# Kernel tuning notes

Measured on AMD Instinct MI355X. Metric: run time of the kernel, lower is better.

The kernel has to match this reference:

```python
import jax, jax.numpy as jnp
import numpy as np

M = 128        # out_features (= in_features here)
N = 20000      # num_node
E = 320000     # num edges (avg degree 16)
KAPPA = 0.99   # inf-norm projection radius (A_rho = 1.0)


def project_linf(W, v):
    """Project each row of W onto the L1 ball of radius v (=> ||W||_inf <= v),
    matching IGNN's projection_norm_inf (rows with L1 norm <= v are untouched)."""
    absW = jnp.abs(W)
    row_l1 = absW.sum(axis=1)
    u = jnp.sort(absW, axis=1)[:, ::-1]          # descending per row
    cssv = jnp.cumsum(u, axis=1) - v
    ind = jnp.arange(1, W.shape[1] + 1, dtype=W.dtype)
    rho = jnp.sum(u * ind > cssv, axis=1)        # support size, >=1 when row_l1 > v
    theta = cssv[jnp.arange(W.shape[0]), rho - 1] / rho.astype(W.dtype)
    proj = jnp.sign(W) * jnp.maximum(absW - theta[:, None], 0.0)
    return jnp.where((row_l1 > v)[:, None], proj, W)


def spmm_right(Xm, rows, cols, vals, n):
    """Compute Xm @ A for sparse A with A[rows[e], cols[e]] = vals[e]; Xm: [m, n]."""
    g = Xm[:, rows] * vals                                    # [m, E]
    return jax.ops.segment_sum(g.T, cols, num_segments=n).T  # [m, n]


def setup_inputs() -> dict:
    key = jax.random.key(0)
    ks = jax.random.split(key, 7)
    stdv = 1.0 / np.sqrt(M)
    X_0 = jax.random.normal(ks[0], (M, N), jnp.float32)
    U = jax.random.normal(ks[1], (M, N), jnp.float32)
    W = jax.random.uniform(ks[2], (M, M), jnp.float32, -stdv, stdv)
    Omega_1 = jax.random.uniform(ks[3], (M, M), jnp.float32, -stdv, stdv)
    A_rows = jax.random.randint(ks[4], (E,), 0, N)
    A_cols = jax.random.randint(ks[5], (E,), 0, N)
    # positive, roughly degree-normalized adjacency values
    A_values = jax.random.uniform(ks[6], (E,), jnp.float32) / 16.0
    return dict(X_0=X_0, U=U, W=W, Omega_1=Omega_1, A_values=A_values,
                A_rows=A_rows, A_cols=A_cols, fw_mitr=30)


def reference(X_0, U, W, Omega_1, A_values, A_rows, A_cols, fw_mitr):
    n = X_0.shape[1]
    # self.W = projection_norm_inf(self.W, kappa / A_rho), A_rho = 1.0
    Wp = project_linf(W, KAPPA)
    # b_Omega = (A^T @ (U^T @ Omega_1^T))^T = (Omega_1 @ U) @ A
    B = spmm_right(Omega_1 @ U, A_rows, A_cols, A_values, n)  # [m, n]
    # ImplicitFunction fixed-point iteration: X <- phi(W @ X @ A + B), phi = relu
    def step(X, _):
        X_new = jax.nn.relu(spmm_right(Wp @ X, A_rows, A_cols, A_values, n) + B)
        return X_new, None
    X, _ = jax.lax.scan(step, X_0, None, length=fw_mitr)
    return X
```

## Files before the change

kernel.cpp:

```cpp
#include <hip/hip_runtime.h>

#define MDIM 128
#define NCOL 20000
#define NEDGE 320000
#define NITER 30
#define FKAPPA 0.99f

typedef unsigned int uint;
typedef unsigned short ushort;
typedef __attribute__((ext_vector_type(8))) short short8;
typedef __attribute__((ext_vector_type(4))) float f32x4;

__device__ __forceinline__ float bf2f(ushort b){
    uint u = ((uint)b) << 16;
    return __builtin_bit_cast(float, u);
}
__device__ __forceinline__ ushort f2bf(float f){
    uint u = __builtin_bit_cast(uint, f);
    uint r = (u + 0x7fffu + ((u >> 16) & 1u)) >> 16;
    return (ushort)r;
}

__global__ void k_zero(int* __restrict__ p){
    int i = blockIdx.x * 256 + threadIdx.x;
    if (i < 2 * NCOL) p[i] = 0;
}

__global__ void k_hist(const int* __restrict__ cols, int* __restrict__ cnt){
    int e = blockIdx.x * 256 + threadIdx.x;
    if (e < NEDGE) atomicAdd(&cnt[cols[e]], 1);
}

__global__ void k_scan(const int* __restrict__ cnt, int* __restrict__ start){
    __shared__ int lds[256];
    const int SEG = (NCOL + 255) / 256;
    int t = threadIdx.x;
    int lo = t * SEG;
    int hi = min(lo + SEG, NCOL);
    int s = 0;
    for (int i = lo; i < hi; ++i) s += cnt[i];
    lds[t] = s;
    __syncthreads();
    for (int off = 1; off < 256; off <<= 1){
        int v = (t >= off) ? lds[t - off] : 0;
        __syncthreads();
        lds[t] += v;
        __syncthreads();
    }
    int run = (t > 0) ? lds[t - 1] : 0;
    for (int i = lo; i < hi; ++i){ start[i] = run; run += cnt[i]; }
    if (hi == NCOL && lo < NCOL) start[NCOL] = run;
}

__global__ void k_scatter(const int* __restrict__ rows, const int* __restrict__ cols,
                          const float* __restrict__ vals, const int* __restrict__ start,
                          int* __restrict__ cursor, uint2* __restrict__ edges){
    int e = blockIdx.x * 256 + threadIdx.x;
    if (e < NEDGE){
        int c = cols[e];
        int p = start[c] + atomicAdd(&cursor[c], 1);
        edges[p] = make_uint2((uint)rows[e], __builtin_bit_cast(uint, vals[e]));
    }
}

__global__ void k_project(const float* __restrict__ W, ushort* __restrict__ Wp){
    int row = blockIdx.x * 4 + (threadIdx.x >> 6);
    int l = threadIdx.x & 63;
    const float* wr = W + row * MDIM;
    float w0 = wr[l], w1 = wr[l + 64];
    float a0 = fabsf(w0), a1 = fabsf(w1);
    float s = a0 + a1, mx = fmaxf(a0, a1);
    for (int off = 32; off; off >>= 1){
        s += __shfl_xor(s, off);
        mx = fmaxf(mx, __shfl_xor(mx, off));
    }
    if (s > FKAPPA){
        float tlo = 0.f, thi = mx;
        for (int it = 0; it < 48; ++it){
            float th = 0.5f * (tlo + thi);
            float f = fmaxf(a0 - th, 0.f) + fmaxf(a1 - th, 0.f);
            for (int off = 32; off; off >>= 1) f += __shfl_xor(f, off);
            if (f > FKAPPA) tlo = th; else thi = th;
        }
        float th = 0.5f * (tlo + thi);
        w0 = copysignf(fmaxf(a0 - th, 0.f), w0);
        w1 = copysignf(fmaxf(a1 - th, 0.f), w1);
    }
    Wp[row * MDIM + l] = f2bf(w0);
    Wp[row * MDIM + l + 64] = f2bf(w1);
}

__global__ void k_cvt(const float* __restrict__ src, ushort* __restrict__ dst){
    int i = blockIdx.x * 256 + threadIdx.x;
    if (i < MDIM * MDIM) dst[i] = f2bf(src[i]);
}

__global__ void k_tin(const float* __restrict__ X0, const float* __restrict__ U,
                      ushort* __restrict__ Xt, ushort* __restrict__ Ut){
    __shared__ ushort tile[128 * 66];
    const float* src = blockIdx.y ? U : X0;
    ushort* dst = blockIdx.y ? Ut : Xt;
    int c0 = blockIdx.x * 64;
    int t = threadIdx.x;
    for (int it = 0; it < 32; ++it){
        int le = it * 256 + t;
        int j = le & 63, m = le >> 6;
        int c = c0 + j;
        tile[m * 66 + j] = (c < NCOL) ? f2bf(src[m * NCOL + c]) : (ushort)0;
    }
    __syncthreads();
    for (int it = 0; it < 32; ++it){
        int le = it * 256 + t;
        int m = le & 127, jc = le >> 7;
        int c = c0 + jc;
        if (c < NCOL) dst[c * MDIM + m] = tile[m * 66 + jc];
    }
}

__global__ void k_tout(const ushort* __restrict__ Xt, float* __restrict__ out){
    __shared__ ushort tile[128 * 66];
    int c0 = blockIdx.x * 64;
    int t = threadIdx.x;
    for (int it = 0; it < 32; ++it){
        int le = it * 256 + t;
        int m = le & 127, jc = le >> 7;
        int c = c0 + jc;
        tile[m * 66 + jc] = (c < NCOL) ? Xt[c * MDIM + m] : (ushort)0;
    }
    __syncthreads();
    for (int it = 0; it < 32; ++it){
        int le = it * 256 + t;
        int j = le & 63, m = le >> 6;
        int c = c0 + j;
        if (c < NCOL) out[m * NCOL + c] = bf2f(tile[m * 66 + j]);
    }
}

__device__ __forceinline__ void fma8(float* acc, uint4 x, float v){
    acc[0] += v * bf2f((ushort)(x.x & 0xffffu)); acc[1] += v * bf2f((ushort)(x.x >> 16));
    acc[2] += v * bf2f((ushort)(x.y & 0xffffu)); acc[3] += v * bf2f((ushort)(x.y >> 16));
    acc[4] += v * bf2f((ushort)(x.z & 0xffffu)); acc[5] += v * bf2f((ushort)(x.z >> 16));
    acc[6] += v * bf2f((ushort)(x.w & 0xffffu)); acc[7] += v * bf2f((ushort)(x.w >> 16));
}

template<int MODE>
__global__ __launch_bounds__(256, 5) void k_fused(const ushort* __restrict__ Xt_in,
                        const ushort* __restrict__ Mat,
                        const ushort* __restrict__ Bt,
                        ushort* __restrict__ outp,
                        const int* __restrict__ start,
                        const uint2* __restrict__ edges){
    __shared__ alignas(16) char GL[4 * 1024];
    int t = threadIdx.x;
    int w = t >> 6, l = t & 63;
    int c0 = blockIdx.x * 16;
    int g = l >> 4;
    int sub = l & 15;

    int sa[5];
    #pragma unroll
    for (int i = 0; i < 5; ++i) sa[i] = start[c0 + w * 4 + i];

    {
        auto preload = [&](int jj) -> uint2 {
            int s = sa[jj], e = sa[jj + 1];
            int idx = (e > s) ? min(s + l, e - 1) : 0;
            return edges[idx];
        };
        uint2 my = preload(0);
        #pragma unroll
        for (int jj = 0; jj < 4; ++jj){
            uint2 nxt = (jj < 3) ? preload(jj + 1) : my;
            int s = sa[jj], e = sa[jj + 1];
            int d = e - s;
            int dd = min(d, 64);
            float acc[8] = {0.f,0.f,0.f,0.f,0.f,0.f,0.f,0.f};
            int k = 0;
            for (; k + 16 <= dd; k += 16){
                int r0 = __shfl((int)my.x, k + g);
                int r1 = __shfl((int)my.x, k + 4 + g);
                int r2 = __shfl((int)my.x, k + 8 + g);
                int r3 = __shfl((int)my.x, k + 12 + g);
                float v0 = __builtin_bit_cast(float, __shfl((int)my.y, k + g));
                float v1 = __builtin_bit_cast(float, __shfl((int)my.y, k + 4 + g));
                float v2 = __builtin_bit_cast(float, __shfl((int)my.y, k + 8 + g));
                float v3 = __builtin_bit_cast(float, __shfl((int)my.y, k + 12 + g));
                uint4 x0 = *(const uint4*)(Xt_in + (size_t)(uint)r0 * 128 + sub * 8);
                uint4 x1 = *(const uint4*)(Xt_in + (size_t)(uint)r1 * 128 + sub * 8);
                uint4 x2 = *(const uint4*)(Xt_in + (size_t)(uint)r2 * 128 + sub * 8);
                uint4 x3 = *(const uint4*)(Xt_in + (size_t)(uint)r3 * 128 + sub * 8);
                fma8(acc, x0, v0); fma8(acc, x1, v1); fma8(acc, x2, v2); fma8(acc, x3, v3);
            }
            for (; k < dd; k += 4){
                int ke = k + g;
                int sel = min(ke, dd - 1);
                int rr = __shfl((int)my.x, sel);
                float vv = __builtin_bit_cast(float, __shfl((int)my.y, sel));
                vv = (ke < dd) ? vv : 0.f;
                uint4 x = *(const uint4*)(Xt_in + (size_t)(uint)rr * 128 + sub * 8);
                fma8(acc, x, vv);
            }
            if (d > 64){
                for (int k2 = sa[jj] + 64; k2 < e; k2 += 4){
                    int ke = k2 + g;
                    uint2 p = edges[min(ke, e - 1)];
                    float vv = (ke < e) ? __builtin_bit_cast(float, p.y) : 0.f;
                    uint4 x = *(const uint4*)(Xt_in + (size_t)p.x * 128 + sub * 8);
                    fma8(acc, x, vv);
                }
            }
            #pragma unroll
            for (int i = 0; i < 8; ++i){
                acc[i] += __shfl_xor(acc[i], 16);
                acc[i] += __shfl_xor(acc[i], 32);
            }
            int j = w * 4 + jj;
            if (l < 16){
                uint4 pk;
                pk.x = (uint)f2bf(acc[0]) | ((uint)f2bf(acc[1]) << 16);
                pk.y = (uint)f2bf(acc[2]) | ((uint)f2bf(acc[3]) << 16);
                pk.z = (uint)f2bf(acc[4]) | ((uint)f2bf(acc[5]) << 16);
                pk.w = (uint)f2bf(acc[6]) | ((uint)f2bf(acc[7]) << 16);
                *(uint4*)(GL + ((j * 256 + sub * 16) ^ ((j & 7) << 4))) = pk;
            }
            my = nxt;
        }
    }

    __builtin_amdgcn_sched_barrier(0);

    short8 bfr[2][4];
    #pragma unroll
    for (int mt = 0; mt < 2; ++mt){
        int m = w * 32 + mt * 16 + (l & 15);
        #pragma unroll
        for (int kc = 0; kc < 4; ++kc)
            bfr[mt][kc] = *(const short8*)(Mat + m * MDIM + kc * 32 + (l >> 4) * 8);
    }
    __syncthreads();

    {
        int arow = l & 15;
        int klane = (l >> 4) * 16;
        int asw = (arow & 7) << 4;
        short8 afr[4];
        #pragma unroll
        for (int kc = 0; kc < 4; ++kc)
            afr[kc] = *(const short8*)(GL + ((arow * 256 + kc * 64 + klane) ^ asw));
        #pragma unroll
        for (int mt = 0; mt < 2; ++mt){
            int m = w * 32 + mt * 16 + (l & 15);
            f32x4 acc4 = {0.f, 0.f, 0.f, 0.f};
            #pragma unroll
            for (int kc = 0; kc < 4; ++kc)
                acc4 = __builtin_amdgcn_mfma_f32_16x16x32_bf16(afr[kc], bfr[mt][kc], acc4, 0, 0, 0);
            int crow_base = c0 + ((l >> 4) << 2);
            #pragma unroll
            for (int q = 0; q < 4; ++q){
                int c = crow_base + q;
                float val = acc4[q];
                if (MODE == 1){
                    val += bf2f(Bt[c * MDIM + m]);
                    val = fmaxf(val, 0.f);
                }
                outp[c * MDIM + m] = f2bf(val);
            }
        }
    }
}

extern "C" void kernel_launch(void* const* d_in, const int* in_sizes, int n_in,
                              void* d_out, int out_size, void* d_ws, size_t ws_size,
                              hipStream_t stream){
    const float* X0 = (const float*)d_in[0];
    const float* U  = (const float*)d_in[1];
    const float* W  = (const float*)d_in[2];
    const float* Om = (const float*)d_in[3];
    const float* Av = (const float*)d_in[4];
    const int*   Ar = (const int*)d_in[5];
    const int*   Ac = (const int*)d_in[6];
    (void)in_sizes; (void)n_in; (void)out_size; (void)ws_size;

    char* ws = (char*)d_ws;
    size_t off = 0;
    auto alloc = [&](size_t bytes) -> char* {
        char* p = ws + off;
        off += (bytes + 255) & ~(size_t)255;
        return p;
    };
    int*    start = (int*)alloc((NCOL + 1) * 4);
    uint2*  edges = (uint2*)alloc(NEDGE * 8);
    ushort* Wp    = (ushort*)alloc(MDIM * MDIM * 2);
    ushort* Omb   = (ushort*)alloc(MDIM * MDIM * 2);
    ushort* P0    = (ushort*)alloc(NCOL * MDIM * 2);

    int* cnt    = (int*)P0;
    int* cursor = cnt + NCOL;

    ushort* P1   = (ushort*)d_out;
    ushort* BtBF = (ushort*)((char*)d_out + NCOL * MDIM * 2);

    k_zero<<<(2 * NCOL + 255) / 256, 256, 0, stream>>>(cnt);
    k_hist<<<(NEDGE + 255) / 256, 256, 0, stream>>>(Ac, cnt);
    k_scan<<<1, 256, 0, stream>>>(cnt, start);
    k_scatter<<<(NEDGE + 255) / 256, 256, 0, stream>>>(Ar, Ac, Av, start, cursor, edges);
    k_project<<<32, 256, 0, stream>>>(W, Wp);
    k_cvt<<<64, 256, 0, stream>>>(Om, Omb);
    k_tin<<<dim3(313, 2), 256, 0, stream>>>(X0, U, P0, P1);
    k_fused<0><<<1250, 256, 0, stream>>>(P1, Omb, nullptr, BtBF, start, edges);
    const ushort* cur = P0; ushort* nxt = P1;
    for (int i = 0; i < NITER; ++i){
        k_fused<1><<<1250, 256, 0, stream>>>(cur, Wp, BtBF, nxt, start, edges);
        ushort* tmp = (ushort*)cur; cur = nxt; nxt = tmp;
    }
    k_tout<<<313, 256, 0, stream>>>(cur, (float*)d_out);
}
```

Before: 622.2 us.

## Double-buffer neighbor row gathers across columns and prefetch bias before MFMA

The per-column gather loop is replaced by a software pipeline. Each wave issues a fixed batch of eight neighbor-row loads for the next column while it accumulates the current one, and the edge records for all four columns are preloaded up front. Bias values for the ReLU epilogue are loaded before the barrier rather than inside the output loop, and the occupancy hint drops from 5 to 4 blocks to make room for the extra registers. The aim is more memory-level parallelism in the latency-bound gather. The cost is redundant clamped loads for low-degree columns, fewer resident waves, and a spill to a slow path for columns with more than 32 edges.

```diff
diff --git a/kernel.cpp b/kernel.cpp
--- a/kernel.cpp
+++ b/kernel.cpp
@@ -144,7 +144,7 @@
 }
 
 template<int MODE>
-__global__ __launch_bounds__(256, 5) void k_fused(const ushort* __restrict__ Xt_in,
+__global__ __launch_bounds__(256, 4) void k_fused(const ushort* __restrict__ Xt_in,
                         const ushort* __restrict__ Mat,
                         const ushort* __restrict__ Bt,
                         ushort* __restrict__ outp,
@@ -161,71 +161,71 @@
     #pragma unroll
     for (int i = 0; i < 5; ++i) sa[i] = start[c0 + w * 4 + i];
 
+    uint2 myv[4];
+    #pragma unroll
+    for (int jj = 0; jj < 4; ++jj){
+        int s = sa[jj], e = sa[jj + 1];
+        int idx = (e > s) ? min(s + l, e - 1) : 0;
+        myv[jj] = edges[idx];
+    }
+
+#define LOADS(X, col) do { \
+    int d_ = sa[(col) + 1] - sa[(col)]; \
+    uint rx_ = myv[(col)].x; \
+    _Pragma("unroll") \
+    for (int r = 0; r < 8; ++r){ \
+        int sel_ = min(r * 4 + g, max(d_ - 1, 0)); \
+        int row_ = __shfl((int)rx_, sel_); \
+        X[r] = *(const uint4*)(Xt_in + (size_t)(uint)row_ * 128 + sub * 8); \
+    } } while (0)
+
+#define PROC(X, col) do { \
+    int s_ = sa[(col)], e_ = sa[(col) + 1]; \
+    int d_ = e_ - s_; \
+    uint ry_ = myv[(col)].y; \
+    float acc[8] = {0.f,0.f,0.f,0.f,0.f,0.f,0.f,0.f}; \
+    _Pragma("unroll") \
+    for (int r = 0; r < 8; ++r){ \
+        int slot_ = r * 4 + g; \
+        int sel_ = min(slot_, max(d_ - 1, 0)); \
+        float v_ = __builtin_bit_cast(float, __shfl((int)ry_, sel_)); \
+        v_ = (slot_ < d_) ? v_ : 0.f; \
+        fma8(acc, X[r], v_); \
+    } \
+    if (d_ > 32){ \
+        for (int k2 = s_ + 32; k2 < e_; k2 += 4){ \
+            int ke_ = k2 + g; \
+            uint2 p_ = edges[min(ke_, e_ - 1)]; \
+            float vv_ = (ke_ < e_) ? __builtin_bit_cast(float, p_.y) : 0.f; \
+            uint4 xx_ = *(const uint4*)(Xt_in + (size_t)p_.x * 128 + sub * 8); \
+            fma8(acc, xx_, vv_); \
+        } \
+    } \
+    _Pragma("unroll") \
+    for (int i = 0; i < 8; ++i){ \
+        acc[i] += __shfl_xor(acc[i], 16); \
+        acc[i] += __shfl_xor(acc[i], 32); \
+    } \
+    int j_ = w * 4 + (col); \
+    if (l < 16){ \
+        uint4 pk_; \
+        pk_.x = (uint)f2bf(acc[0]) | ((uint)f2bf(acc[1]) << 16); \
+        pk_.y = (uint)f2bf(acc[2]) | ((uint)f2bf(acc[3]) << 16); \
+        pk_.z = (uint)f2bf(acc[4]) | ((uint)f2bf(acc[5]) << 16); \
+        pk_.w = (uint)f2bf(acc[6]) | ((uint)f2bf(acc[7]) << 16); \
+        *(uint4*)(GL + ((j_ * 256 + sub * 16) ^ ((j_ & 7) << 4))) = pk_; \
+    } } while (0)
+
     {
-        auto preload = [&](int jj) -> uint2 {
-            int s = sa[jj], e = sa[jj + 1];
-            int idx = (e > s) ? min(s + l, e - 1) : 0;
-            return edges[idx];
-        };
-        uint2 my = preload(0);
-        #pragma unroll
-        for (int jj = 0; jj < 4; ++jj){
-            uint2 nxt = (jj < 3) ? preload(jj + 1) : my;
-            int s = sa[jj], e = sa[jj + 1];
-            int d = e - s;
-            int dd = min(d, 64);
-            float acc[8] = {0.f,0.f,0.f,0.f,0.f,0.f,0.f,0.f};
-            int k = 0;
-            for (; k + 16 <= dd; k += 16){
-                int r0 = __shfl((int)my.x, k + g);
-                int r1 = __shfl((int)my.x, k + 4 + g);
-                int r2 = __shfl((int)my.x, k + 8 + g);
-                int r3 = __shfl((int)my.x, k + 12 + g);
-                float v0 = __builtin_bit_cast(float, __shfl((int)my.y, k + g));
-                float v1 = __builtin_bit_cast(float, __shfl((int)my.y, k + 4 + g));
-                float v2 = __builtin_bit_cast(float, __shfl((int)my.y, k + 8 + g));
-                float v3 = __builtin_bit_cast(float, __shfl((int)my.y, k + 12 + g));
-                uint4 x0 = *(const uint4*)(Xt_in + (size_t)(uint)r0 * 128 + sub * 8);
-                uint4 x1 = *(const uint4*)(Xt_in + (size_t)(uint)r1 * 128 + sub * 8);
-                uint4 x2 = *(const uint4*)(Xt_in + (size_t)(uint)r2 * 128 + sub * 8);
-                uint4 x3 = *(const uint4*)(Xt_in + (size_t)(uint)r3 * 128 + sub * 8);
-                fma8(acc, x0, v0); fma8(acc, x1, v1); fma8(acc, x2, v2); fma8(acc, x3, v3);
-            }
-            for (; k < dd; k += 4){
-                int ke = k + g;
-                int sel = min(ke, dd - 1);
-                int rr = __shfl((int)my.x, sel);
-                float vv = __builtin_bit_cast(float, __shfl((int)my.y, sel));
-                vv = (ke < dd) ? vv : 0.f;
-                uint4 x = *(const uint4*)(Xt_in + (size_t)(uint)rr * 128 + sub * 8);
-                fma8(acc, x, vv);
-            }
-            if (d > 64){
-                for (int k2 = sa[jj] + 64; k2 < e; k2 += 4){
-                    int ke = k2 + g;
-                    uint2 p = edges[min(ke, e - 1)];
-                    float vv = (ke < e) ? __builtin_bit_cast(float, p.y) : 0.f;
-                    uint4 x = *(const uint4*)(Xt_in + (size_t)p.x * 128 + sub * 8);
-                    fma8(acc, x, vv);
-                }
-            }
-            #pragma unroll
-            for (int i = 0; i < 8; ++i){
-                acc[i] += __shfl_xor(acc[i], 16);
-                acc[i] += __shfl_xor(acc[i], 32);
-            }
-            int j = w * 4 + jj;
-            if (l < 16){
-                uint4 pk;
-                pk.x = (uint)f2bf(acc[0]) | ((uint)f2bf(acc[1]) << 16);
-                pk.y = (uint)f2bf(acc[2]) | ((uint)f2bf(acc[3]) << 16);
-                pk.z = (uint)f2bf(acc[4]) | ((uint)f2bf(acc[5]) << 16);
-                pk.w = (uint)f2bf(acc[6]) | ((uint)f2bf(acc[7]) << 16);
-                *(uint4*)(GL + ((j * 256 + sub * 16) ^ ((j & 7) << 4))) = pk;
-            }
-            my = nxt;
-        }
-    }
+        uint4 xa[8], xb[8];
+        LOADS(xa, 0);
+        LOADS(xb, 1); PROC(xa, 0);
+        LOADS(xa, 2); PROC(xb, 1);
+        LOADS(xb, 3); PROC(xa, 2);
+        PROC(xb, 3);
+    }
+#undef LOADS
+#undef PROC
 
     __builtin_amdgcn_sched_barrier(0);
 
@@ -236,6 +236,23 @@
         #pragma unroll
         for (int kc = 0; kc < 4; ++kc)
             bfr[mt][kc] = *(const short8*)(Mat + m * MDIM + kc * 32 + (l >> 4) * 8);
+    }
+
+    float btv[2][2][4];
+    if (MODE == 1){
+        #pragma unroll
+        for (int cw = 0; cw < 2; ++cw){
+            #pragma unroll
+            for (int mt = 0; mt < 2; ++mt){
+                int m = w * 32 + mt * 16 + (l & 15);
+                #pragma unroll
+                for (int q = 0; q < 4; ++q){
+                    int cl = cw * 8 + ((l >> 4) << 1) + (q >> 1);
+                    (void)cl;
+                    btv[cw][mt][q] = bf2f(Bt[(size_t)(c0 + cw * 16 + ((l >> 4) << 2) + q) * MDIM + m]);
+                }
+            }
+        }
     }
     __syncthreads();
 
@@ -260,8 +277,7 @@
                 int c = crow_base + q;
                 float val = acc4[q];
                 if (MODE == 1){
-                    val += bf2f(Bt[c * MDIM + m]);
-                    val = fmaxf(val, 0.f);
+                    val = fmaxf(val + btv[0][mt][q], 0.f);
                 }
                 outp[c * MDIM + m] = f2bf(val);
             }
```

Measured after the change: 736.7 us. +18.4%, slower.
